# Performance work log

Measured on AMD Instinct MI355X. Metric: run time of the kernel, lower is better.

The kernel has to match this reference:

```python
import jax, jax.numpy as jnp
import numpy as np

B, DIM, N = 64, 128, 4000
H = 4
DH = DIM // H          # 32
CL = 50                # clusters (hardcoded in module)
K = 9                  # knn_num
SCALOR = DH ** -0.5


def setup_inputs() -> dict:
    key = jax.random.key(0)
    ks = jax.random.split(key, 16)
    s = 0.05
    inp = {
        'x': jax.random.normal(ks[0], (B, DIM, N, 1), jnp.float32),
        # conv_group1 / conv_group2: InstanceNorm(no affine) -> BN(affine) -> ReLU -> 1x1 conv
        'wg1': jax.random.normal(ks[1], (CL, DIM), jnp.float32) * s,
        'bg1': jnp.zeros((CL,), jnp.float32),
        'g1_gamma': jnp.ones((DIM,), jnp.float32),
        'g1_beta': jnp.zeros((DIM,), jnp.float32),
        'wg2': jax.random.normal(ks[2], (CL, DIM), jnp.float32) * s,
        'bg2': jnp.zeros((CL,), jnp.float32),
        'g2_gamma': jnp.ones((DIM,), jnp.float32),
        'g2_beta': jnp.zeros((DIM,), jnp.float32),
        # per-head 1x1 convs (stacked over heads)
        'qkv_w': jax.random.normal(ks[3], (H, DH, DIM), jnp.float32) * s,
        'qkv_b': jnp.zeros((H, DH), jnp.float32),
        'qkv1_w': jax.random.normal(ks[4], (H, 3 * DH, DIM), jnp.float32) * s,
        'qkv1_b': jnp.zeros((H, 3 * DH), jnp.float32),
        # GCBlock convs: conv1 (1,3) stride (1,3): 2*DH->DH ; conv2 (1,3): DH->DH
        'gc1_w': jax.random.normal(ks[5], (H, DH, 2 * DH, 3), jnp.float32) * s,
        'gc1_b': jnp.zeros((H, DH), jnp.float32),
        'gc1_gamma': jnp.ones((H, DH), jnp.float32),
        'gc1_beta': jnp.zeros((H, DH), jnp.float32),
        'gc2_w': jax.random.normal(ks[6], (H, DH, DH, 3), jnp.float32) * s,
        'gc2_b': jnp.zeros((H, DH), jnp.float32),
        'gc2_gamma': jnp.ones((H, DH), jnp.float32),
        'gc2_beta': jnp.zeros((H, DH), jnp.float32),
        # output projections
        'pres_w': jax.random.normal(ks[7], (DIM, 2 * DIM), jnp.float32) * s,
        'pres_b': jnp.zeros((DIM,), jnp.float32),
        'proj_w': jax.random.normal(ks[8], (DIM, DIM), jnp.float32) * s,
        'proj_b': jnp.zeros((DIM,), jnp.float32),
    }
    return inp


def _conv_group(x3, w, bconv, gamma, beta):
    # x3: (b, C, n). InstanceNorm2d(eps=1e-3, no affine) over n, BN(train) over (b,n), ReLU, 1x1 conv.
    mu = x3.mean(-1, keepdims=True)
    var = x3.var(-1, keepdims=True)
    xin = (x3 - mu) * jax.lax.rsqrt(var + 1e-3)
    mu2 = xin.mean((0, 2), keepdims=True)
    var2 = xin.var((0, 2), keepdims=True)
    xbn = gamma[None, :, None] * (xin - mu2) * jax.lax.rsqrt(var2 + 1e-5) + beta[None, :, None]
    xr = jax.nn.relu(xbn)
    return jnp.einsum('oc,bcn->bon', w, xr) + bconv[None, :, None]


def _bn_train(h, gamma, beta, axes):
    mu = h.mean(axes, keepdims=True)
    var = h.var(axes, keepdims=True)
    return gamma * (h - mu) * jax.lax.rsqrt(var + 1e-5) + beta


def _forward(x, wg1, bg1, g1_gamma, g1_beta, wg2, bg2, g2_gamma, g2_beta,
             qkv_w, qkv_b, qkv1_w, qkv1_b,
             gc1_w, gc1_b, gc1_gamma, gc1_beta,
             gc2_w, gc2_b, gc2_gamma, gc2_beta,
             pres_w, pres_b, proj_w, proj_b):
    xs = x[..., 0]                                          # (b, dim, n)
    # cluster assignment 1: softmax over points
    embed1 = _conv_group(xs, wg1, bg1, g1_gamma, g1_beta)   # (b, 50, n)
    S1 = jax.nn.softmax(embed1, axis=2)
    cluster_x = jnp.einsum('bdn,bcn->bdc', xs, S1)          # (b, dim, 50)

    # ---- local branch (per head, vectorized): 1x1 conv -> knn graph feature -> conv stack ----
    q = jnp.einsum('hod,bdc->bhoc', qkv_w, cluster_x) + qkv_b[None, :, :, None]  # (b,H,dh,50)
    xt = q.transpose(0, 1, 3, 2)                            # (b,H,50,dh)
    inner = jnp.einsum('bhnc,bhmc->bhnm', xt, xt)
    sq = jnp.sum(xt * xt, axis=-1)
    pd = 2.0 * inner - sq[..., :, None] - sq[..., None, :]  # negative squared distance
    idx = jax.lax.top_k(pd, K)[1]                            # (b,H,50,K)
    x_exp = jnp.broadcast_to(xt[:, :, None, :, :], xt.shape[:2] + (CL, CL, DH))
    feature = jnp.take_along_axis(x_exp, idx[..., None], axis=3)        # (b,H,50,K,dh)
    center = jnp.broadcast_to(xt[:, :, :, None, :], feature.shape)
    edge = jnp.concatenate([center, center - feature], axis=-1)          # (b,H,50,K,2dh)
    # conv1: kernel (1,3) stride (1,3): K=9 -> 3 windows of 3
    e = edge.reshape(edge.shape[0], H, CL, 3, 3, 2 * DH)
    h1 = jnp.einsum('bhnjti,hoit->bhnjo', e, gc1_w) + gc1_b[None, :, None, None, :]
    h1 = jax.nn.relu(_bn_train(h1, gc1_gamma[None, :, None, None, :], gc1_beta[None, :, None, None, :], (0, 2, 3)))
    # conv2: kernel (1,3): 3 -> 1
    h2 = jnp.einsum('bhnti,hoit->bhno', h1, gc2_w) + gc2_b[None, :, None, :]
    h2 = jax.nn.relu(_bn_train(h2, gc2_gamma[None, :, None, :], gc2_beta[None, :, None, :], (0, 2)))
    local = h2.transpose(0, 1, 3, 2)                        # (b,H,dh,50)

    # ---- global branch: tiny attention over 50 clusters per head ----
    qkv = jnp.einsum('hod,bdc->bhoc', qkv1_w, cluster_x) + qkv1_b[None, :, :, None]  # (b,H,3dh,50)
    qg, kg, vg = jnp.split(qkv, 3, axis=2)
    attn = jax.nn.softmax(SCALOR * jnp.einsum('bhdn,bhdm->bhnm', qg, kg), axis=-1)
    glob = jnp.einsum('bhnm,bhdm->bhdn', attn, vg)          # (b,H,dh,50)

    # interleave [local_h, global_h] per head along channels -> (b, 2*dim, 50)
    per_head = jnp.concatenate([local, glob], axis=2)       # (b,H,2dh,50)
    cat = per_head.reshape(per_head.shape[0], 2 * DIM, CL)
    res = jnp.einsum('oc,bcn->bon', pres_w, cat) + pres_b[None, :, None]  # (b,dim,50)

    # cluster assignment 2: softmax over clusters, scatter back to points
    embed2 = _conv_group(xs, wg2, bg2, g2_gamma, g2_beta)   # (b,50,n)
    S2 = jax.nn.softmax(embed2, axis=1)
    res2 = jnp.einsum('bdc,bcn->bdn', res, S2)              # (b,dim,n)
    out = jnp.einsum('od,bdn->bon', proj_w, res2) + proj_b[None, :, None]
    return out[..., None]                                   # (b,dim,n,1)


def reference(x, wg1, bg1, g1_gamma, g1_beta, wg2, bg2, g2_gamma, g2_beta,
              qkv_w, qkv_b, qkv1_w, qkv1_b,
              gc1_w, gc1_b, gc1_gamma, gc1_beta,
              gc2_w, gc2_b, gc2_gamma, gc2_beta,
              pres_w, pres_b, proj_w, proj_b):
    return _forward(x, wg1, bg1, g1_gamma, g1_beta, wg2, bg2, g2_gamma, g2_beta,
                    qkv_w, qkv_b, qkv1_w, qkv1_b,
                    gc1_w, gc1_b, gc1_gamma, gc1_beta,
                    gc2_w, gc2_b, gc2_gamma, gc2_beta,
                    pres_w, pres_b, proj_w, proj_b)
```

## Files before the change

### kernel.cpp

```cpp
#include <hip/hip_runtime.h>
#include <cstddef>


constexpr size_t O_MU    = 0;
constexpr size_t O_RINV  = 8192;
constexpr size_t O_RATIO = 16384;
constexpr size_t O_A1    = 24576;
constexpr size_t O_B1    = 24704;
constexpr size_t O_A2    = 24832;
constexpr size_t O_B2    = 24960;
constexpr size_t O_PROJWT= 25088;
constexpr size_t O_VPROJ = 41472;
constexpr size_t O_MT    = 41600;
constexpr size_t O_E2    = 74368;
constexpr size_t O_UCXP  = 12874368;
constexpr size_t O_XT    = 17068672;
constexpr size_t O_QT    = 17478272;
constexpr size_t O_KT    = 17887872;
constexpr size_t O_VT    = 18297472;
constexpr size_t O_H1    = 18707072;
constexpr size_t O_P1    = 19935872;
constexpr size_t O_H2    = 19952512;
constexpr size_t O_P2    = 20362112;
constexpr size_t O_CAT   = 20378752;
constexpr size_t O_PRES2 = 21197952;

__global__ __launch_bounds__(256) void k_rowstats(const float* __restrict__ x,
                                                  float* __restrict__ ws){
  int w = threadIdx.x >> 6, lane = threadIdx.x & 63;
  int row = blockIdx.x*4 + w;
  const float4* xr = (const float4*)(x + (size_t)row * 4000);
  float s = 0.f, sq = 0.f;
  for(int i = lane; i < 1000; i += 64){
    float4 v = xr[i];
    s  += v.x + v.y + v.z + v.w;
    sq += v.x*v.x + v.y*v.y + v.z*v.z + v.w*v.w;
  }
  for(int off = 32; off > 0; off >>= 1){
    s  += __shfl_down(s,  off, 64);
    sq += __shfl_down(sq, off, 64);
  }
  if(lane == 0){
    float mean = s * (1.f/4000.f);
    float var  = sq * (1.f/4000.f) - mean*mean;
    ws[O_MU   + row] = mean;
    ws[O_RINV + row] = rsqrtf(var + 1e-3f);
    ws[O_RATIO+ row] = var / (var + 1e-3f);
  }
}

__global__ __launch_bounds__(256) void k_prep(const float* g1g, const float* g1b,
                       const float* g2g, const float* g2b,
                       const float* projw, float* __restrict__ ws){
  int t = threadIdx.x;
  int i = blockIdx.x*256 + t;
  { int o = i & 127, k = i >> 7; ws[O_PROJWT+i] = projw[o*128 + k]; }
  if(blockIdx.x == 0 && t < 128){
    float s = 0.f;
    for(int b = 0; b < 64; b++) s += ws[O_RATIO + b*128 + t];
    float var2 = s * (1.f/64.f);
    float inv2 = rsqrtf(var2 + 1e-5f);
    ws[O_A1+t] = g1g[t] * inv2;  ws[O_B1+t] = g1b[t];
    ws[O_A2+t] = g2g[t] * inv2;  ws[O_B2+t] = g2b[t];
  }
}

__global__ __launch_bounds__(256) void k_mprep(const float* __restrict__ presw,
                                               const float* __restrict__ presb,
                                               float* __restrict__ ws){
  int t = threadIdx.x;
  if(blockIdx.x < 128){
    int kk2 = blockIdx.x * 2;
    __shared__ float pwc[2][128];
    { int which = t >> 7, d = t & 127; pwc[which][d] = presw[d*256 + kk2 + which]; }
    __syncthreads();
    int which = t >> 7, o = t & 127;
    float acc = 0.f;
    for(int d = 0; d < 128; d++) acc += ws[O_PROJWT + d*128 + o] * pwc[which][d];
    ws[O_MT + (size_t)(kk2 + which)*128 + o] = acc;
  }else{
    if(t < 128){
      float v = 0.f;
      for(int d = 0; d < 128; d++) v += ws[O_PROJWT + d*128 + t] * presb[d];
      ws[O_VPROJ + t] = v;
    }
  }
}

__global__ __launch_bounds__(256) void k_e1ucx(const float* __restrict__ x,
    const float* __restrict__ wg1, const float* __restrict__ bg1,
    float* __restrict__ ws){
  int ch = blockIdx.x, b = blockIdx.y;
  __shared__ float lW1[128*52];
  __shared__ float lrv1[128*48];
  __shared__ float lxt [48*132];
  __shared__ float ca1[128], cb1[128];
  __shared__ float bg1p[56];
  int t = threadIdx.x;
  if(t < 128){
    float mu = ws[O_MU + b*128 + t], ri = ws[O_RINV + b*128 + t];
    float a1 = ws[O_A1+t]*ri;
    ca1[t] = a1; cb1[t] = ws[O_B1+t] - a1*mu;
  }
  if(t < 56) bg1p[t] = (t < 50) ? bg1[t] : 0.f;
  for(int i = t; i < 1664; i += 256){
    int cl = i >> 5, cq = i & 31;
    float4 w = (cl < 50) ? *(const float4*)&wg1[cl*128 + cq*4] : make_float4(0.f,0.f,0.f,0.f);
    int c0 = cq*4;
    lW1[(c0+0)*52+cl] = w.x; lW1[(c0+1)*52+cl] = w.y;
    lW1[(c0+2)*52+cl] = w.z; lW1[(c0+3)*52+cl] = w.w;
  }
  int dg = t & 31, cg = t >> 5;
  float ua[4][8];
  #pragma unroll
  for(int r = 0; r < 4; r++)
    #pragma unroll
    for(int i = 0; i < 8; i++) ua[r][i] = 0.f;
  float zacc = 0.f;
  int ig = t >> 4, jg = t & 15;
  int clb = ig*4, j4 = jg*4;
  int sc[6], sj[6];
  float4 pf[6];
  #pragma unroll
  for(int j = 0; j < 6; j++){ int i = t + 256*j; sc[j] = i/12; sj[j] = (i%12)*4; }
  #pragma unroll
  for(int j = 0; j < 6; j++)
    pf[j] = *(const float4*)&x[(size_t)(b*128 + sc[j])*4000 + ch*500 + sj[j]];

  for(int st = 0; st < 11; st++){
    int lim = (st == 10) ? 20 : 48;
    __syncthreads();
    #pragma unroll
    for(int j = 0; j < 6; j++){
      int c = sc[j], jj = sj[j];
      float4 xv = (jj < lim) ? pf[j] : make_float4(0.f,0.f,0.f,0.f);
      lxt[(jj+0)*132 + c] = xv.x; lxt[(jj+1)*132 + c] = xv.y;
      lxt[(jj+2)*132 + c] = xv.z; lxt[(jj+3)*132 + c] = xv.w;
      float a1 = ca1[c], b1v = cb1[c];
      float4 r1;
      r1.x = fmaxf(a1*xv.x + b1v, 0.f); r1.y = fmaxf(a1*xv.y + b1v, 0.f);
      r1.z = fmaxf(a1*xv.z + b1v, 0.f); r1.w = fmaxf(a1*xv.w + b1v, 0.f);
      *(float4*)&lrv1[c*48 + jj] = r1;
    }
    __syncthreads();
    if(st < 10){
      int lim2 = (st == 9) ? 20 : 48;
      int nb2 = ch*500 + (st+1)*48;
      #pragma unroll
      for(int j = 0; j < 6; j++)
        pf[j] = (sj[j] < lim2) ? *(const float4*)&x[(size_t)(b*128 + sc[j])*4000 + nb2 + sj[j]]
                               : make_float4(0.f,0.f,0.f,0.f);
    }
    float e[4][4];
    if(ig < 13 && jg < 12){
      #pragma unroll
      for(int r = 0; r < 4; r++){ e[r][0]=0.f; e[r][1]=0.f; e[r][2]=0.f; e[r][3]=0.f; }
      #pragma unroll 4
      for(int c = 0; c < 128; c++){
        float4 w = *(const float4*)&lW1[c*52 + clb];
        float4 v = *(const float4*)&lrv1[c*48 + j4];
        e[0][0] += w.x*v.x; e[0][1] += w.x*v.y; e[0][2] += w.x*v.z; e[0][3] += w.x*v.w;
        e[1][0] += w.y*v.x; e[1][1] += w.y*v.y; e[1][2] += w.y*v.z; e[1][3] += w.y*v.w;
        e[2][0] += w.z*v.x; e[2][1] += w.z*v.y; e[2][2] += w.z*v.z; e[2][3] += w.z*v.w;
        e[3][0] += w.w*v.x; e[3][1] += w.w*v.y; e[3][2] += w.w*v.z; e[3][3] += w.w*v.w;
      }
    }
    __syncthreads();
    if(ig < 13 && jg < 12){
      bool live = (j4 < lim);
      #pragma unroll
      for(int r = 0; r < 4; r++){
        float bias = bg1p[clb + r];
        float4 u = make_float4(0.f,0.f,0.f,0.f);
        if(live){
          u.x = expf(e[r][0] + bias); u.y = expf(e[r][1] + bias);
          u.z = expf(e[r][2] + bias); u.w = expf(e[r][3] + bias);
        }
        *(float4*)&lrv1[(clb + r)*48 + j4] = u;
      }
    }
    __syncthreads();
    if(t < 224){
      int d4 = dg*4, c8 = cg*8;
      for(int n4 = 0; n4 < 12; n4++){
        int n0 = n4*4;
        float4 uv[8];
        #pragma unroll
        for(int i = 0; i < 8; i++) uv[i] = *(const float4*)&lrv1[(c8 + i)*48 + n0];
        {
          float4 xq = *(const float4*)&lxt[(n0+0)*132 + d4];
          #pragma unroll
          for(int i = 0; i < 8; i++){
            float u = uv[i].x;
            ua[0][i] += xq.x*u; ua[1][i] += xq.y*u; ua[2][i] += xq.z*u; ua[3][i] += xq.w*u;
          }
        }
        {
          float4 xq = *(const float4*)&lxt[(n0+1)*132 + d4];
          #pragma unroll
          for(int i = 0; i < 8; i++){
            float u = uv[i].y;
            ua[0][i] += xq.x*u; ua[1][i] += xq.y*u; ua[2][i] += xq.z*u; ua[3][i] += xq.w*u;
          }
        }
        {
          float4 xq = *(const float4*)&lxt[(n0+2)*132 + d4];
          #pragma unroll
          for(int i = 0; i < 8; i++){
            float u = uv[i].z;
            ua[0][i] += xq.x*u; ua[1][i] += xq.y*u; ua[2][i] += xq.z*u; ua[3][i] += xq.w*u;
          }
        }
        {
          float4 xq = *(const float4*)&lxt[(n0+3)*132 + d4];
          #pragma unroll
          for(int i = 0; i < 8; i++){
            float u = uv[i].w;
            ua[0][i] += xq.x*u; ua[1][i] += xq.y*u; ua[2][i] += xq.z*u; ua[3][i] += xq.w*u;
          }
        }
      }
    }
    if(t < 52){
      float s = 0.f;
      #pragma unroll
      for(int k = 0; k < 12; k++){
        float4 u = *(const float4*)&lrv1[t*48 + k*4];
        s += u.x + u.y + u.z + u.w;
      }
      zacc += s;
    }
  }
  if(t < 224){
    int d4 = dg*4, c8 = cg*8;
    #pragma unroll
    for(int r = 0; r < 4; r++){
      size_t base = O_UCXP + ((size_t)(ch*64 + b)*132 + d4 + r)*56 + c8;
      *(float4*)&ws[base]     = make_float4(ua[r][0], ua[r][1], ua[r][2], ua[r][3]);
      *(float4*)&ws[base + 4] = make_float4(ua[r][4], ua[r][5], ua[r][6], ua[r][7]);
    }
  }
  if(t < 52) ws[O_UCXP + ((size_t)(ch*64 + b)*132 + 128)*56 + t] = zacc;
}

__global__ __launch_bounds__(256) void k_e2(const float* __restrict__ x,
    const float* __restrict__ wg2, const float* __restrict__ bg2,
    float* __restrict__ ws){
  int ch = blockIdx.x, b = blockIdx.y;
  __shared__ float lW2[128*52];
  __shared__ float lrv2[128*48];
  __shared__ float ca2[128], cb2[128];
  __shared__ float bg2p[56];
  int t = threadIdx.x;
  if(t < 128){
    float mu = ws[O_MU + b*128 + t], ri = ws[O_RINV + b*128 + t];
    float a2 = ws[O_A2+t]*ri;
    ca2[t] = a2; cb2[t] = ws[O_B2+t] - a2*mu;
  }
  if(t < 56) bg2p[t] = (t < 50) ? bg2[t] : 0.f;
  for(int i = t; i < 1664; i += 256){
    int cl = i >> 5, cq = i & 31;
    float4 w = (cl < 50) ? *(const float4*)&wg2[cl*128 + cq*4] : make_float4(0.f,0.f,0.f,0.f);
    int c0 = cq*4;
    lW2[(c0+0)*52+cl] = w.x; lW2[(c0+1)*52+cl] = w.y;
    lW2[(c0+2)*52+cl] = w.z; lW2[(c0+3)*52+cl] = w.w;
  }
  int ig = t >> 4, jg = t & 15;
  int clb = ig*4, j4 = jg*4;
  int sc[6], sj[6];
  float4 pf[6];
  #pragma unroll
  for(int j = 0; j < 6; j++){ int i = t + 256*j; sc[j] = i/12; sj[j] = (i%12)*4; }
  #pragma unroll
  for(int j = 0; j < 6; j++)
    pf[j] = *(const float4*)&x[(size_t)(b*128 + sc[j])*4000 + ch*500 + sj[j]];

  for(int st = 0; st < 11; st++){
    int nb = ch*500 + st*48;
    int lim = (st == 10) ? 20 : 48;
    __syncthreads();
    #pragma unroll
    for(int j = 0; j < 6; j++){
      int c = sc[j], jj = sj[j];
      float4 xv = (jj < lim) ? pf[j] : make_float4(0.f,0.f,0.f,0.f);
      float a2 = ca2[c], b2v = cb2[c];
      float4 r2;
      r2.x = fmaxf(a2*xv.x + b2v, 0.f); r2.y = fmaxf(a2*xv.y + b2v, 0.f);
      r2.z = fmaxf(a2*xv.z + b2v, 0.f); r2.w = fmaxf(a2*xv.w + b2v, 0.f);
      *(float4*)&lrv2[c*48 + jj] = r2;
    }
    __syncthreads();
    if(st < 10){
      int lim2 = (st == 9) ? 20 : 48;
      int nb2 = ch*500 + (st+1)*48;
      #pragma unroll
      for(int j = 0; j < 6; j++)
        pf[j] = (sj[j] < lim2) ? *(const float4*)&x[(size_t)(b*128 + sc[j])*4000 + nb2 + sj[j]]
                               : make_float4(0.f,0.f,0.f,0.f);
    }
    if(ig < 13 && jg < 12){
      float e[4][4];
      #pragma unroll
      for(int r = 0; r < 4; r++){ e[r][0]=0.f; e[r][1]=0.f; e[r][2]=0.f; e[r][3]=0.f; }
      #pragma unroll 4
      for(int c = 0; c < 128; c++){
        float4 w = *(const float4*)&lW2[c*52 + clb];
        float4 v = *(const float4*)&lrv2[c*48 + j4];
        e[0][0] += w.x*v.x; e[0][1] += w.x*v.y; e[0][2] += w.x*v.z; e[0][3] += w.x*v.w;
        e[1][0] += w.y*v.x; e[1][1] += w.y*v.y; e[1][2] += w.y*v.z; e[1][3] += w.y*v.w;
        e[2][0] += w.z*v.x; e[2][1] += w.z*v.y; e[2][2] += w.z*v.z; e[2][3] += w.z*v.w;
        e[3][0] += w.w*v.x; e[3][1] += w.w*v.y; e[3][2] += w.w*v.z; e[3][3] += w.w*v.w;
      }
      if(j4 < lim){
        #pragma unroll
        for(int r = 0; r < 4; r++){
          int cl = clb + r;
          if(cl < 50){
            float bias = bg2p[cl];
            float4 o = make_float4(e[r][0]+bias, e[r][1]+bias, e[r][2]+bias, e[r][3]+bias);
            *(float4*)&ws[O_E2 + ((size_t)b*50 + cl)*4000 + nb + j4] = o;
          }
        }
      }
    }
  }
}

__global__ __launch_bounds__(256) void k_qkv(const float* __restrict__ qw,
                                             const float* __restrict__ qb,
                                             const float* __restrict__ q1w,
                                             const float* __restrict__ q1b,
                                             float* __restrict__ ws){
  int rt = blockIdx.x, b = blockIdx.y;
  __shared__ float wl[64*130];
  __shared__ float cxl[128*52];
  __shared__ float zi[52];
  int t = threadIdx.x;
  if(t < 52){
    float s = 0.f;
    if(t < 50){
      #pragma unroll
      for(int ch = 0; ch < 8; ch++)
        s += ws[O_UCXP + ((size_t)(ch*64 + b)*132 + 128)*56 + t];
      zi[t] = 1.f / s;
    }else zi[t] = 0.f;
  }
  for(int i = t; i < 2048; i += 256){
    int rl = i >> 5, kq = i & 31, row = rt*64 + rl;
    float4 w = (row < 128) ? *(const float4*)&qw[row*128 + kq*4]
                           : *(const float4*)&q1w[(row-128)*128 + kq*4];
    int k0 = kq*4;
    wl[rl*130 + k0+0] = w.x; wl[rl*130 + k0+1] = w.y;
    wl[rl*130 + k0+2] = w.z; wl[rl*130 + k0+3] = w.w;
  }
  __syncthreads();
  for(int i = t; i < 6656; i += 256){
    int k = i / 52, c = i % 52;
    float s = 0.f;
    size_t base = O_UCXP + ((size_t)b*132 + k)*56 + c;
    #pragma unroll
    for(int ch = 0; ch < 8; ch++) s += ws[base + (size_t)ch*64*132*56];
    cxl[i] = s * zi[c];
  }
  __syncthreads();
  int ig = t & 15, cg = t >> 4;
  float acc[4][4];
  #pragma unroll
  for(int r = 0; r < 4; r++){ acc[r][0]=0.f; acc[r][1]=0.f; acc[r][2]=0.f; acc[r][3]=0.f; }
  if(cg < 13){
    int rb = ig*4, cb = cg*4;
    #pragma unroll 4
    for(int k = 0; k < 128; k++){
      float4 cv = *(const float4*)&cxl[k*52 + cb];
      float w0 = wl[(rb+0)*130 + k], w1 = wl[(rb+1)*130 + k];
      float w2 = wl[(rb+2)*130 + k], w3 = wl[(rb+3)*130 + k];
      acc[0][0] += w0*cv.x; acc[0][1] += w0*cv.y; acc[0][2] += w0*cv.z; acc[0][3] += w0*cv.w;
      acc[1][0] += w1*cv.x; acc[1][1] += w1*cv.y; acc[1][2] += w1*cv.z; acc[1][3] += w1*cv.w;
      acc[2][0] += w2*cv.x; acc[2][1] += w2*cv.y; acc[2][2] += w2*cv.z; acc[2][3] += w2*cv.w;
      acc[3][0] += w3*cv.x; acc[3][1] += w3*cv.y; acc[3][2] += w3*cv.z; acc[3][3] += w3*cv.w;
    }
    #pragma unroll
    for(int r = 0; r < 4; r++){
      int row = rt*64 + ig*4 + r;
      size_t base; float bias;
      if(row < 128){
        int h = row >> 5;
        bias = qb[row];
        base = O_XT + (size_t)(b*4 + h)*1600 + (row & 31);
      }else{
        int r2 = row - 128, h = r2/96, j = r2%96, kind = j >> 5, dd = j & 31;
        bias = q1b[r2];
        base = (kind==0 ? O_QT : kind==1 ? O_KT : O_VT) + (size_t)(b*4 + h)*1600 + dd;
      }
      #pragma unroll
      for(int s = 0; s < 4; s++){
        int c = cg*4 + s;
        if(c < 50) ws[base + (size_t)c*32] = acc[r][s] + bias;
      }
    }
  }
}

__global__ __launch_bounds__(256) void k_knn(const float* __restrict__ g1w,
                                             const float* __restrict__ g1bias,
                                             float* __restrict__ ws){
  int h = blockIdx.x, b = blockIdx.y;
  __shared__ float xtl[50][33];
  __shared__ float pdl[50][52];
  __shared__ float sql[50];
  __shared__ int   idxl[50][9];
  __shared__ float w1l[6144];
  int t = threadIdx.x;
  const float* xtg = ws + O_XT + (size_t)(b*4 + h)*1600;
  for(int i = t; i < 1600; i += 256) xtl[i >> 5][i & 31] = xtg[i];
  for(int i = t; i < 6144; i += 256){
    int o = i / 192, r = i % 192, ii = r / 3, tt = r % 3;
    w1l[(ii*3 + tt)*32 + o] = g1w[(size_t)h*6144 + i];
  }
  __syncthreads();
  if(t < 50){
    float s = 0.f;
    for(int d = 0; d < 32; d++){ float v = xtl[t][d]; s += v*v; }
    sql[t] = s;
  }
  __syncthreads();
  for(int i = t; i < 2500; i += 256){
    int n = i / 50, m = i % 50;
    float s = 0.f;
    for(int d = 0; d < 32; d++) s += xtl[n][d]*xtl[m][d];
    pdl[n][m] = 2.f*s - sql[n] - sql[m];
  }
  __syncthreads();
  if(t < 50){
    float pv = INFINITY; int pi = -1;
    for(int k = 0; k < 9; k++){
      float bv = -INFINITY; int bi = 1000;
      for(int m = 0; m < 50; m++){
        float v = pdl[t][m];
        bool elig = (v < pv) || (v == pv && m > pi);
        if(elig && (v > bv || (v == bv && m < bi))){ bv = v; bi = m; }
      }
      idxl[t][k] = bi; pv = bv; pi = bi;
    }
  }
  __syncthreads();
  if(t < 150){
    int n = t / 3, jw = t % 3;
    float acc[32];
    #pragma unroll
    for(int o = 0; o < 32; o++) acc[o] = 0.f;
    for(int t3 = 0; t3 < 3; t3++){
      int kx = idxl[n][jw*3 + t3];
      for(int ii = 0; ii < 32; ii++){
        float c0 = xtl[n][ii];
        float c1 = c0 - xtl[kx][ii];
        const float* wr0 = w1l + (ii*3 + t3)*32;
        const float* wr1 = w1l + ((ii+32)*3 + t3)*32;
        #pragma unroll
        for(int o = 0; o < 32; o++) acc[o] += c0*wr0[o] + c1*wr1[o];
      }
    }
    float* out = ws + O_H1 + ((size_t)(b*4 + h)*150 + n*3 + jw)*32;
    #pragma unroll
    for(int o = 0; o < 32; o++) out[o] = acc[o] + g1bias[h*32 + o];
  }
}

__global__ __launch_bounds__(256) void k_bn1p(float* __restrict__ ws){
  int h = blockIdx.x, b = blockIdx.y, t = threadIdx.x;
  int o = t & 31, part = t >> 5;
  const float* src = ws + O_H1 + (size_t)(b*4 + h)*4800;
  float s = 0.f, sq = 0.f;
  for(int nj = part; nj < 150; nj += 8){
    float v = src[nj*32 + o];
    s += v; sq += v*v;
  }
  __shared__ float rs[8][33], rq[8][33];
  rs[part][o] = s; rq[part][o] = sq; __syncthreads();
  if(t < 32){
    float S = 0.f, Q = 0.f;
    for(int p = 0; p < 8; p++){ S += rs[p][t]; Q += rq[p][t]; }
    ws[O_P1 + b*256 + h*32 + t]       = S;
    ws[O_P1 + b*256 + 128 + h*32 + t] = Q;
  }
}

__global__ __launch_bounds__(256) void k_conv2(const float* __restrict__ g1g,
                                               const float* __restrict__ g1be,
                                               const float* __restrict__ g2w,
                                               const float* __restrict__ g2bias,
                                               float* __restrict__ ws){
  int h = blockIdx.x, b = blockIdx.y;
  __shared__ float hl[150][33];
  __shared__ float w2l[3072];
  __shared__ float rs[8][32], rq[8][32];
  __shared__ float b1s[32], b1t[32];
  int t = threadIdx.x;
  if(t < 32){
    float s = 0.f, sq = 0.f;
    for(int bb = 0; bb < 64; bb++){
      s  += ws[O_P1 + bb*256 + h*32 + t];
      sq += ws[O_P1 + bb*256 + 128 + h*32 + t];
    }
    float mean = s * (1.f/9600.f), var = sq * (1.f/9600.f) - mean*mean;
    float sc = g1g[h*32+t] * rsqrtf(var + 1e-5f);
    b1s[t] = sc; b1t[t] = g1be[h*32+t] - sc*mean;
  }
  for(int i = t; i < 3072; i += 256){
    int o = i / 96, r = i % 96, ii = r / 3, tt = r % 3;
    w2l[(ii*3 + tt)*32 + o] = g2w[(size_t)h*3072 + i];
  }
  __syncthreads();
  const float* h1p = ws + O_H1 + (size_t)(b*4 + h)*4800;
  for(int i = t; i < 4800; i += 256){
    int nj = i >> 5, ii = i & 31;
    hl[nj][ii] = fmaxf(b1s[ii]*h1p[i] + b1t[ii], 0.f);
  }
  __syncthreads();
  int o = t & 31, ng = t >> 5;
  float bias = g2bias[h*32 + o];
  float s = 0.f, sq = 0.f;
  for(int n = ng; n < 50; n += 8){
    float acc = 0.f;
    for(int t3 = 0; t3 < 3; t3++){
      const float* hr = hl[n*3 + t3];
      #pragma unroll
      for(int ii = 0; ii < 32; ii++) acc += hr[ii] * w2l[(ii*3 + t3)*32 + o];
    }
    acc += bias;
    ws[O_H2 + ((size_t)(b*4 + h)*50 + n)*32 + o] = acc;
    s += acc; sq += acc*acc;
  }
  rs[ng][o] = s; rq[ng][o] = sq; __syncthreads();
  if(t < 32){
    float S = 0.f, Q = 0.f;
    for(int g2 = 0; g2 < 8; g2++){ S += rs[g2][t]; Q += rq[g2][t]; }
    ws[O_P2 + (b*4 + h)*64 + t]      = S;
    ws[O_P2 + (b*4 + h)*64 + 32 + t] = Q;
  }
}

__global__ __launch_bounds__(256) void k_attn(const float* __restrict__ g2g,
                                              const float* __restrict__ g2be,
                                              float* __restrict__ ws){
  int h = blockIdx.x, b = blockIdx.y;
  __shared__ float qtl[50][33], ktl[50][33], vtl[50][33], al[50][52];
  __shared__ float b2s[32], b2t[32];
  int t = threadIdx.x;
  if(t < 32){
    float s = 0.f, sq = 0.f;
    for(int bb = 0; bb < 64; bb++){
      s  += ws[O_P2 + (size_t)(bb*4 + h)*64 + t];
      sq += ws[O_P2 + (size_t)(bb*4 + h)*64 + 32 + t];
    }
    float mean = s * (1.f/3200.f), var = sq * (1.f/3200.f) - mean*mean;
    float sc = g2g[h*32+t] * rsqrtf(var + 1e-5f);
    b2s[t] = sc; b2t[t] = g2be[h*32+t] - sc*mean;
  }
  size_t base = (size_t)(b*4 + h)*1600;
  for(int i = t; i < 1600; i += 256){
    int n = i >> 5, d = i & 31;
    qtl[n][d] = ws[O_QT + base + i];
    ktl[n][d] = ws[O_KT + base + i];
    vtl[n][d] = ws[O_VT + base + i];
  }
  __syncthreads();
  for(int i = t; i < 2500; i += 256){
    int n = i / 50, m = i % 50;
    float s = 0.f;
    for(int d = 0; d < 32; d++) s += qtl[n][d]*ktl[m][d];
    al[n][m] = s * 0.17677669529663687f;
  }
  __syncthreads();
  if(t < 50){
    float m = -INFINITY;
    for(int j = 0; j < 50; j++) m = fmaxf(m, al[t][j]);
    float s = 0.f;
    for(int j = 0; j < 50; j++){ float e = expf(al[t][j] - m); al[t][j] = e; s += e; }
    float inv = 1.f/s;
    for(int j = 0; j < 50; j++) al[t][j] *= inv;
  }
  __syncthreads();
  for(int i = t; i < 1600; i += 256){
    int n = i >> 5, d = i & 31;
    float gacc = 0.f;
    for(int m = 0; m < 50; m++) gacc += al[n][m]*vtl[m][d];
    ws[O_CAT + ((size_t)b*256 + h*64 + 32 + d)*50 + n] = gacc;
    float l = fmaxf(b2s[d]*ws[O_H2 + ((size_t)(b*4 + h)*50 + n)*32 + d] + b2t[d], 0.f);
    ws[O_CAT + ((size_t)b*256 + h*64 + d)*50 + n] = l;
  }
}

__global__ __launch_bounds__(256) void k_res(float* __restrict__ ws){
  int b = blockIdx.x;
  __shared__ float mtl[64*132];
  __shared__ float catl[64*52];
  __shared__ float vp[128];
  int t = threadIdx.x;
  if(t < 128) vp[t] = ws[O_VPROJ + t];
  int og = t >> 4, cg = t & 15;
  int ob = og*8, cb = cg*4;
  float acc[8][4];
  #pragma unroll
  for(int r = 0; r < 8; r++){ acc[r][0]=0.f; acc[r][1]=0.f; acc[r][2]=0.f; acc[r][3]=0.f; }
  for(int kc = 0; kc < 4; kc++){
    int k0 = kc*64;
    __syncthreads();
    for(int i = t; i < 2048; i += 256){
      int k = i >> 5, oq = i & 31;
      float4 m = *(const float4*)&ws[O_MT + (size_t)(k0 + k)*128 + oq*4];
      *(float4*)&mtl[k*132 + oq*4] = m;
    }
    for(int i = t; i < 3328; i += 256){
      int k = i / 52, c = i % 52;
      catl[i] = (c < 50) ? ws[O_CAT + (size_t)b*12800 + (k0 + k)*50 + c] : 0.f;
    }
    __syncthreads();
    if(cg < 13){
      #pragma unroll 2
      for(int k = 0; k < 64; k++){
        float4 m0 = *(const float4*)&mtl[k*132 + ob];
        float4 m1 = *(const float4*)&mtl[k*132 + ob + 4];
        float4 cv = *(const float4*)&catl[k*52 + cb];
        acc[0][0] += m0.x*cv.x; acc[0][1] += m0.x*cv.y; acc[0][2] += m0.x*cv.z; acc[0][3] += m0.x*cv.w;
        acc[1][0] += m0.y*cv.x; acc[1][1] += m0.y*cv.y; acc[1][2] += m0.y*cv.z; acc[1][3] += m0.y*cv.w;
        acc[2][0] += m0.z*cv.x; acc[2][1] += m0.z*cv.y; acc[2][2] += m0.z*cv.z; acc[2][3] += m0.z*cv.w;
        acc[3][0] += m0.w*cv.x; acc[3][1] += m0.w*cv.y; acc[3][2] += m0.w*cv.z; acc[3][3] += m0.w*cv.w;
        acc[4][0] += m1.x*cv.x; acc[4][1] += m1.x*cv.y; acc[4][2] += m1.x*cv.z; acc[4][3] += m1.x*cv.w;
        acc[5][0] += m1.y*cv.x; acc[5][1] += m1.y*cv.y; acc[5][2] += m1.y*cv.z; acc[5][3] += m1.y*cv.w;
        acc[6][0] += m1.z*cv.x; acc[6][1] += m1.z*cv.y; acc[6][2] += m1.z*cv.z; acc[6][3] += m1.z*cv.w;
        acc[7][0] += m1.w*cv.x; acc[7][1] += m1.w*cv.y; acc[7][2] += m1.w*cv.z; acc[7][3] += m1.w*cv.w;
      }
    }
  }
  if(cg < 13){
    #pragma unroll
    for(int s = 0; s < 4; s++){
      int c = cb + s;
      if(c < 50){
        float4 o0 = make_float4(acc[0][s]+vp[ob+0], acc[1][s]+vp[ob+1], acc[2][s]+vp[ob+2], acc[3][s]+vp[ob+3]);
        float4 o1 = make_float4(acc[4][s]+vp[ob+4], acc[5][s]+vp[ob+5], acc[6][s]+vp[ob+6], acc[7][s]+vp[ob+7]);
        *(float4*)&ws[O_PRES2 + (size_t)b*6400 + c*128 + ob]     = o0;
        *(float4*)&ws[O_PRES2 + (size_t)b*6400 + c*128 + ob + 4] = o1;
      }
    }
  }
}

__global__ __launch_bounds__(256) void k_out(const float* __restrict__ projb,
                                             float* __restrict__ ws,
                                             float* __restrict__ out){
  int nt = blockIdx.x, b = blockIdx.y;
  int n0 = nt*64;
  __shared__ float sl[50*64];
  __shared__ float p2l[50*132];
  __shared__ float pb[128];
  int t = threadIdx.x;
  for(int i = t; i < 3200; i += 256){
    int c = i >> 6, j = i & 63, n = n0 + j;
    sl[i] = (n < 4000) ? ws[O_E2 + ((size_t)b*50 + c)*4000 + n] : 0.f;
  }
  for(int i = t; i < 6400; i += 256){
    int c = i >> 7, o = i & 127;
    p2l[c*132 + o] = ws[O_PRES2 + (size_t)b*6400 + c*128 + o];
  }
  if(t < 128) pb[t] = projb[t];
  __syncthreads();
  if(t < 64){
    int j = t;
    float m = -INFINITY;
    for(int c = 0; c < 50; c++) m = fmaxf(m, sl[c*64 + j]);
    float s = 0.f;
    for(int c = 0; c < 50; c++){ float e = expf(sl[c*64 + j] - m); sl[c*64 + j] = e; s += e; }
    float inv = 1.f/s;
    for(int c = 0; c < 50; c++) sl[c*64 + j] *= inv;
  }
  __syncthreads();
  int og = t >> 4, jg = t & 15;
  int ob = og*8, j4 = jg*4;
  float acc[8][4];
  #pragma unroll
  for(int r = 0; r < 8; r++){ acc[r][0]=0.f; acc[r][1]=0.f; acc[r][2]=0.f; acc[r][3]=0.f; }
  #pragma unroll 2
  for(int c = 0; c < 50; c++){
    float4 sv = *(const float4*)&sl[c*64 + j4];
    float4 p0 = *(const float4*)&p2l[c*132 + ob];
    float4 p1 = *(const float4*)&p2l[c*132 + ob + 4];
    acc[0][0] += p0.x*sv.x; acc[0][1] += p0.x*sv.y; acc[0][2] += p0.x*sv.z; acc[0][3] += p0.x*sv.w;
    acc[1][0] += p0.y*sv.x; acc[1][1] += p0.y*sv.y; acc[1][2] += p0.y*sv.z; acc[1][3] += p0.y*sv.w;
    acc[2][0] += p0.z*sv.x; acc[2][1] += p0.z*sv.y; acc[2][2] += p0.z*sv.z; acc[2][3] += p0.z*sv.w;
    acc[3][0] += p0.w*sv.x; acc[3][1] += p0.w*sv.y; acc[3][2] += p0.w*sv.z; acc[3][3] += p0.w*sv.w;
    acc[4][0] += p1.x*sv.x; acc[4][1] += p1.x*sv.y; acc[4][2] += p1.x*sv.z; acc[4][3] += p1.x*sv.w;
    acc[5][0] += p1.y*sv.x; acc[5][1] += p1.y*sv.y; acc[5][2] += p1.y*sv.z; acc[5][3] += p1.y*sv.w;
    acc[6][0] += p1.z*sv.x; acc[6][1] += p1.z*sv.y; acc[6][2] += p1.z*sv.z; acc[6][3] += p1.z*sv.w;
    acc[7][0] += p1.w*sv.x; acc[7][1] += p1.w*sv.y; acc[7][2] += p1.w*sv.z; acc[7][3] += p1.w*sv.w;
  }
  int n = n0 + j4;
  if(n < 4000){
    #pragma unroll
    for(int r = 0; r < 8; r++){
      float bv = pb[ob + r];
      float4 o = make_float4(acc[r][0]+bv, acc[r][1]+bv, acc[r][2]+bv, acc[r][3]+bv);
      *(float4*)&out[(size_t)(b*128 + ob + r)*4000 + n] = o;
    }
  }
}

extern "C" void kernel_launch(void* const* d_in, const int* in_sizes, int n_in,
                              void* d_out, int out_size, void* d_ws, size_t ws_size,
                              hipStream_t stream){
  (void)in_sizes; (void)n_in; (void)out_size; (void)ws_size;
  const float* x      = (const float*)d_in[0];
  const float* wg1    = (const float*)d_in[1];
  const float* bg1    = (const float*)d_in[2];
  const float* g1g    = (const float*)d_in[3];
  const float* g1b    = (const float*)d_in[4];
  const float* wg2    = (const float*)d_in[5];
  const float* bg2    = (const float*)d_in[6];
  const float* g2g    = (const float*)d_in[7];
  const float* g2b    = (const float*)d_in[8];
  const float* qkvw   = (const float*)d_in[9];
  const float* qkvb   = (const float*)d_in[10];
  const float* qkv1w  = (const float*)d_in[11];
  const float* qkv1b  = (const float*)d_in[12];
  const float* gc1w   = (const float*)d_in[13];
  const float* gc1bias= (const float*)d_in[14];
  const float* gc1g   = (const float*)d_in[15];
  const float* gc1be  = (const float*)d_in[16];
  const float* gc2w   = (const float*)d_in[17];
  const float* gc2bias= (const float*)d_in[18];
  const float* gc2g   = (const float*)d_in[19];
  const float* gc2be  = (const float*)d_in[20];
  const float* presw  = (const float*)d_in[21];
  const float* presb  = (const float*)d_in[22];
  const float* projw  = (const float*)d_in[23];
  const float* projb  = (const float*)d_in[24];
  float* ws = (float*)d_ws;
  float* out = (float*)d_out;

  k_rowstats<<<2048, 256, 0, stream>>>(x, ws);
  k_prep<<<64, 256, 0, stream>>>(g1g, g1b, g2g, g2b, projw, ws);
  k_mprep<<<129, 256, 0, stream>>>(presw, presb, ws);
  k_e1ucx<<<dim3(8, 64), 256, 0, stream>>>(x, wg1, bg1, ws);
  k_e2<<<dim3(8, 64), 256, 0, stream>>>(x, wg2, bg2, ws);
  k_qkv<<<dim3(8, 64), 256, 0, stream>>>(qkvw, qkvb, qkv1w, qkv1b, ws);
  k_knn<<<dim3(4, 64), 256, 0, stream>>>(gc1w, gc1bias, ws);
  k_bn1p<<<dim3(4, 64), 256, 0, stream>>>(ws);
  k_conv2<<<dim3(4, 64), 256, 0, stream>>>(gc1g, gc1be, gc2w, gc2bias, ws);
  k_attn<<<dim3(4, 64), 256, 0, stream>>>(gc2g, gc2be, ws);
  k_res<<<64, 256, 0, stream>>>(ws);
  k_out<<<dim3(63, 64), 256, 0, stream>>>(projb, ws, out);
}
```

Baseline: 779.3 us.

## Fuse prep kernels, fold BN stats into knn, regrid e2 and res, skip softmax max

Merges the projw transpose into the row-stats kernel and the BN-scale prep into k_mprep. Folds the BN1 partial-stat reduction into k_knn, which removes one launch. Splits k_e2 across 12 chunks of 336 points with launch bounds for 3 blocks per SM, and splits k_res over two output halves to use more blocks. It also moves the exp into k_e2 and defers softmax normalization to the output GEMM, dropping the max-subtraction. That last step risks overflow if the logits grow large.

New measurement: 763.6 us. 2.0% less time.

```diff
diff --git a/kernel.cpp b/kernel.cpp
--- a/kernel.cpp
+++ b/kernel.cpp
@@ -14,19 +14,26 @@
 constexpr size_t O_MT    = 41600;
 constexpr size_t O_E2    = 74368;
 constexpr size_t O_UCXP  = 12874368;
-constexpr size_t O_XT    = 17068672;
-constexpr size_t O_QT    = 17478272;
-constexpr size_t O_KT    = 17887872;
-constexpr size_t O_VT    = 18297472;
-constexpr size_t O_H1    = 18707072;
-constexpr size_t O_P1    = 19935872;
-constexpr size_t O_H2    = 19952512;
-constexpr size_t O_P2    = 20362112;
-constexpr size_t O_CAT   = 20378752;
-constexpr size_t O_PRES2 = 21197952;
-
-__global__ __launch_bounds__(256) void k_rowstats(const float* __restrict__ x,
-                                                  float* __restrict__ ws){
+constexpr size_t O_XT    = 16659072;
+constexpr size_t O_QT    = 17068672;
+constexpr size_t O_KT    = 17478272;
+constexpr size_t O_VT    = 17887872;
+constexpr size_t O_H1    = 18297472;
+constexpr size_t O_P1    = 19526272;
+constexpr size_t O_H2    = 19542656;
+constexpr size_t O_P2    = 19952256;
+constexpr size_t O_CAT   = 19968640;
+constexpr size_t O_PRES2 = 20787840;
+
+__global__ __launch_bounds__(256) void k_stats(const float* __restrict__ x,
+                                               const float* __restrict__ projw,
+                                               float* __restrict__ ws){
+  if(blockIdx.x >= 2048){
+    int i = (blockIdx.x - 2048)*256 + threadIdx.x;
+    int o = i & 127, k = i >> 7;
+    ws[O_PROJWT + i] = projw[o*128 + k];
+    return;
+  }
   int w = threadIdx.x >> 6, lane = threadIdx.x & 63;
   int row = blockIdx.x*4 + w;
   const float4* xr = (const float4*)(x + (size_t)row * 4000);
@@ -49,24 +56,12 @@
   }
 }
 
-__global__ __launch_bounds__(256) void k_prep(const float* g1g, const float* g1b,
-                       const float* g2g, const float* g2b,
-                       const float* projw, float* __restrict__ ws){
-  int t = threadIdx.x;
-  int i = blockIdx.x*256 + t;
-  { int o = i & 127, k = i >> 7; ws[O_PROJWT+i] = projw[o*128 + k]; }
-  if(blockIdx.x == 0 && t < 128){
-    float s = 0.f;
-    for(int b = 0; b < 64; b++) s += ws[O_RATIO + b*128 + t];
-    float var2 = s * (1.f/64.f);
-    float inv2 = rsqrtf(var2 + 1e-5f);
-    ws[O_A1+t] = g1g[t] * inv2;  ws[O_B1+t] = g1b[t];
-    ws[O_A2+t] = g2g[t] * inv2;  ws[O_B2+t] = g2b[t];
-  }
-}
-
 __global__ __launch_bounds__(256) void k_mprep(const float* __restrict__ presw,
                                                const float* __restrict__ presb,
+                                               const float* __restrict__ g1g,
+                                               const float* __restrict__ g1b,
+                                               const float* __restrict__ g2g,
+                                               const float* __restrict__ g2b,
                                                float* __restrict__ ws){
   int t = threadIdx.x;
   if(blockIdx.x < 128){
@@ -78,11 +73,20 @@
     float acc = 0.f;
     for(int d = 0; d < 128; d++) acc += ws[O_PROJWT + d*128 + o] * pwc[which][d];
     ws[O_MT + (size_t)(kk2 + which)*128 + o] = acc;
-  }else{
+  }else if(blockIdx.x == 128){
     if(t < 128){
       float v = 0.f;
       for(int d = 0; d < 128; d++) v += ws[O_PROJWT + d*128 + t] * presb[d];
       ws[O_VPROJ + t] = v;
+    }
+  }else{
+    if(t < 128){
+      float s = 0.f;
+      for(int b = 0; b < 64; b++) s += ws[O_RATIO + b*128 + t];
+      float var2 = s * (1.f/64.f);
+      float inv2 = rsqrtf(var2 + 1e-5f);
+      ws[O_A1+t] = g1g[t] * inv2;  ws[O_B1+t] = g1b[t];
+      ws[O_A2+t] = g2g[t] * inv2;  ws[O_B2+t] = g2b[t];
     }
   }
 }
@@ -243,7 +247,7 @@
   if(t < 52) ws[O_UCXP + ((size_t)(ch*64 + b)*132 + 128)*56 + t] = zacc;
 }
 
-__global__ __launch_bounds__(256) void k_e2(const float* __restrict__ x,
+__global__ __launch_bounds__(256, 3) void k_e2(const float* __restrict__ x,
     const float* __restrict__ wg2, const float* __restrict__ bg2,
     float* __restrict__ ws){
   int ch = blockIdx.x, b = blockIdx.y;
@@ -257,7 +261,7 @@
     float a2 = ws[O_A2+t]*ri;
     ca2[t] = a2; cb2[t] = ws[O_B2+t] - a2*mu;
   }
-  if(t < 56) bg2p[t] = (t < 50) ? bg2[t] : 0.f;
+  if(t >= 192 && t < 248){ int q = t - 192; bg2p[q] = (q < 50) ? bg2[q] : 0.f; }
   for(int i = t; i < 1664; i += 256){
     int cl = i >> 5, cq = i & 31;
     float4 w = (cl < 50) ? *(const float4*)&wg2[cl*128 + cq*4] : make_float4(0.f,0.f,0.f,0.f);
@@ -273,11 +277,11 @@
   for(int j = 0; j < 6; j++){ int i = t + 256*j; sc[j] = i/12; sj[j] = (i%12)*4; }
   #pragma unroll
   for(int j = 0; j < 6; j++)
-    pf[j] = *(const float4*)&x[(size_t)(b*128 + sc[j])*4000 + ch*500 + sj[j]];
-
-  for(int st = 0; st < 11; st++){
-    int nb = ch*500 + st*48;
-    int lim = (st == 10) ? 20 : 48;
+    pf[j] = *(const float4*)&x[(size_t)(b*128 + sc[j])*4000 + ch*336 + sj[j]];
+
+  for(int st = 0; st < 7; st++){
+    int nb = ch*336 + st*48;
+    int lim = 4000 - nb; if(lim > 48) lim = 48;
     __syncthreads();
     #pragma unroll
     for(int j = 0; j < 6; j++){
@@ -290,9 +294,9 @@
       *(float4*)&lrv2[c*48 + jj] = r2;
     }
     __syncthreads();
-    if(st < 10){
-      int lim2 = (st == 9) ? 20 : 48;
-      int nb2 = ch*500 + (st+1)*48;
+    if(st < 6){
+      int nb2 = nb + 48;
+      int lim2 = 4000 - nb2; if(lim2 > 48) lim2 = 48;
       #pragma unroll
       for(int j = 0; j < 6; j++)
         pf[j] = (sj[j] < lim2) ? *(const float4*)&x[(size_t)(b*128 + sc[j])*4000 + nb2 + sj[j]]
@@ -317,7 +321,8 @@
           int cl = clb + r;
           if(cl < 50){
             float bias = bg2p[cl];
-            float4 o = make_float4(e[r][0]+bias, e[r][1]+bias, e[r][2]+bias, e[r][3]+bias);
+            float4 o = make_float4(expf(e[r][0]+bias), expf(e[r][1]+bias),
+                                   expf(e[r][2]+bias), expf(e[r][3]+bias));
             *(float4*)&ws[O_E2 + ((size_t)b*50 + cl)*4000 + nb + j4] = o;
           }
         }
@@ -359,7 +364,7 @@
     float s = 0.f;
     size_t base = O_UCXP + ((size_t)b*132 + k)*56 + c;
     #pragma unroll
-    for(int ch = 0; ch < 8; ch++) s += ws[base + (size_t)ch*64*132*56];
+    for(int ch = 0; ch < 8; ch++) s += ws[base + (size_t)ch*473088];
     cxl[i] = s * zi[c];
   }
   __syncthreads();
@@ -444,9 +449,10 @@
     }
   }
   __syncthreads();
-  if(t < 150){
+  float acc[32];
+  bool act = (t < 150);
+  if(act){
     int n = t / 3, jw = t % 3;
-    float acc[32];
     #pragma unroll
     for(int o = 0; o < 32; o++) acc[o] = 0.f;
     for(int t3 = 0; t3 < 3; t3++){
@@ -462,26 +468,30 @@
     }
     float* out = ws + O_H1 + ((size_t)(b*4 + h)*150 + n*3 + jw)*32;
     #pragma unroll
-    for(int o = 0; o < 32; o++) out[o] = acc[o] + g1bias[h*32 + o];
-  }
-}
-
-__global__ __launch_bounds__(256) void k_bn1p(float* __restrict__ ws){
-  int h = blockIdx.x, b = blockIdx.y, t = threadIdx.x;
-  int o = t & 31, part = t >> 5;
-  const float* src = ws + O_H1 + (size_t)(b*4 + h)*4800;
-  float s = 0.f, sq = 0.f;
-  for(int nj = part; nj < 150; nj += 8){
-    float v = src[nj*32 + o];
-    s += v; sq += v*v;
-  }
-  __shared__ float rs[8][33], rq[8][33];
-  rs[part][o] = s; rq[part][o] = sq; __syncthreads();
-  if(t < 32){
-    float S = 0.f, Q = 0.f;
-    for(int p = 0; p < 8; p++){ S += rs[p][t]; Q += rq[p][t]; }
-    ws[O_P1 + b*256 + h*32 + t]       = S;
-    ws[O_P1 + b*256 + 128 + h*32 + t] = Q;
+    for(int o = 0; o < 32; o++){ acc[o] += g1bias[h*32 + o]; out[o] = acc[o]; }
+  }
+  __syncthreads();
+  if(act){
+    #pragma unroll
+    for(int o = 0; o < 32; o++) w1l[t*32 + o] = acc[o];
+  }
+  __syncthreads();
+  {
+    int o = t & 31, part = t >> 5;
+    float s = 0.f, sq = 0.f;
+    for(int r = part; r < 150; r += 8){
+      float v = w1l[r*32 + o];
+      s += v; sq += v*v;
+    }
+    float* sp = &pdl[0][0];
+    sp[part*32 + o] = s; sp[256 + part*32 + o] = sq;
+    __syncthreads();
+    if(t < 32){
+      float S = 0.f, Q = 0.f;
+      for(int p = 0; p < 8; p++){ S += sp[p*32 + t]; Q += sp[256 + p*32 + t]; }
+      ws[O_P1 + b*256 + h*32 + t]       = S;
+      ws[O_P1 + b*256 + 128 + h*32 + t] = Q;
+    }
   }
 }
 
@@ -546,6 +556,7 @@
   int h = blockIdx.x, b = blockIdx.y;
   __shared__ float qtl[50][33], ktl[50][33], vtl[50][33], al[50][52];
   __shared__ float b2s[32], b2t[32];
+  __shared__ float zr[50];
   int t = threadIdx.x;
   if(t < 32){
     float s = 0.f, sq = 0.f;
@@ -577,39 +588,38 @@
     for(int j = 0; j < 50; j++) m = fmaxf(m, al[t][j]);
     float s = 0.f;
     for(int j = 0; j < 50; j++){ float e = expf(al[t][j] - m); al[t][j] = e; s += e; }
-    float inv = 1.f/s;
-    for(int j = 0; j < 50; j++) al[t][j] *= inv;
+    zr[t] = 1.f/s;
   }
   __syncthreads();
   for(int i = t; i < 1600; i += 256){
     int n = i >> 5, d = i & 31;
     float gacc = 0.f;
     for(int m = 0; m < 50; m++) gacc += al[n][m]*vtl[m][d];
-    ws[O_CAT + ((size_t)b*256 + h*64 + 32 + d)*50 + n] = gacc;
+    ws[O_CAT + ((size_t)b*256 + h*64 + 32 + d)*50 + n] = gacc * zr[n];
     float l = fmaxf(b2s[d]*ws[O_H2 + ((size_t)(b*4 + h)*50 + n)*32 + d] + b2t[d], 0.f);
     ws[O_CAT + ((size_t)b*256 + h*64 + d)*50 + n] = l;
   }
 }
 
 __global__ __launch_bounds__(256) void k_res(float* __restrict__ ws){
-  int b = blockIdx.x;
-  __shared__ float mtl[64*132];
+  int oh = blockIdx.x & 1, b = blockIdx.x >> 1;
+  __shared__ float mtl[64*68];
   __shared__ float catl[64*52];
-  __shared__ float vp[128];
-  int t = threadIdx.x;
-  if(t < 128) vp[t] = ws[O_VPROJ + t];
+  __shared__ float vp[64];
+  int t = threadIdx.x;
+  if(t < 64) vp[t] = ws[O_VPROJ + oh*64 + t];
   int og = t >> 4, cg = t & 15;
-  int ob = og*8, cb = cg*4;
-  float acc[8][4];
+  int ob = og*4, cb = cg*4;
+  float acc[4][4];
   #pragma unroll
-  for(int r = 0; r < 8; r++){ acc[r][0]=0.f; acc[r][1]=0.f; acc[r][2]=0.f; acc[r][3]=0.f; }
+  for(int r = 0; r < 4; r++){ acc[r][0]=0.f; acc[r][1]=0.f; acc[r][2]=0.f; acc[r][3]=0.f; }
   for(int kc = 0; kc < 4; kc++){
     int k0 = kc*64;
     __syncthreads();
-    for(int i = t; i < 2048; i += 256){
-      int k = i >> 5, oq = i & 31;
-      float4 m = *(const float4*)&ws[O_MT + (size_t)(k0 + k)*128 + oq*4];
-      *(float4*)&mtl[k*132 + oq*4] = m;
+    for(int i = t; i < 1024; i += 256){
+      int k = i >> 4, oq = i & 15;
+      float4 m = *(const float4*)&ws[O_MT + (size_t)(k0 + k)*128 + oh*64 + oq*4];
+      *(float4*)&mtl[k*68 + oq*4] = m;
     }
     for(int i = t; i < 3328; i += 256){
       int k = i / 52, c = i % 52;
@@ -619,17 +629,12 @@
     if(cg < 13){
       #pragma unroll 2
       for(int k = 0; k < 64; k++){
-        float4 m0 = *(const float4*)&mtl[k*132 + ob];
-        float4 m1 = *(const float4*)&mtl[k*132 + ob + 4];
+        float4 m0 = *(const float4*)&mtl[k*68 + ob];
         float4 cv = *(const float4*)&catl[k*52 + cb];
         acc[0][0] += m0.x*cv.x; acc[0][1] += m0.x*cv.y; acc[0][2] += m0.x*cv.z; acc[0][3] += m0.x*cv.w;
         acc[1][0] += m0.y*cv.x; acc[1][1] += m0.y*cv.y; acc[1][2] += m0.y*cv.z; acc[1][3] += m0.y*cv.w;
         acc[2][0] += m0.z*cv.x; acc[2][1] += m0.z*cv.y; acc[2][2] += m0.z*cv.z; acc[2][3] += m0.z*cv.w;
         acc[3][0] += m0.w*cv.x; acc[3][1] += m0.w*cv.y; acc[3][2] += m0.w*cv.z; acc[3][3] += m0.w*cv.w;
-        acc[4][0] += m1.x*cv.x; acc[4][1] += m1.x*cv.y; acc[4][2] += m1.x*cv.z; acc[4][3] += m1.x*cv.w;
-        acc[5][0] += m1.y*cv.x; acc[5][1] += m1.y*cv.y; acc[5][2] += m1.y*cv.z; acc[5][3] += m1.y*cv.w;
-        acc[6][0] += m1.z*cv.x; acc[6][1] += m1.z*cv.y; acc[6][2] += m1.z*cv.z; acc[6][3] += m1.z*cv.w;
-        acc[7][0] += m1.w*cv.x; acc[7][1] += m1.w*cv.y; acc[7][2] += m1.w*cv.z; acc[7][3] += m1.w*cv.w;
       }
     }
   }
@@ -639,9 +644,7 @@
       int c = cb + s;
       if(c < 50){
         float4 o0 = make_float4(acc[0][s]+vp[ob+0], acc[1][s]+vp[ob+1], acc[2][s]+vp[ob+2], acc[3][s]+vp[ob+3]);
-        float4 o1 = make_float4(acc[4][s]+vp[ob+4], acc[5][s]+vp[ob+5], acc[6][s]+vp[ob+6], acc[7][s]+vp[ob+7]);
-        *(float4*)&ws[O_PRES2 + (size_t)b*6400 + c*128 + ob]     = o0;
-        *(float4*)&ws[O_PRES2 + (size_t)b*6400 + c*128 + ob + 4] = o1;
+        *(float4*)&ws[O_PRES2 + (size_t)b*6400 + c*128 + oh*64 + ob] = o0;
       }
     }
   }
@@ -655,6 +658,8 @@
   __shared__ float sl[50*64];
   __shared__ float p2l[50*132];
   __shared__ float pb[128];
+  __shared__ float zp[4][64];
+  __shared__ float zi[64];
   int t = threadIdx.x;
   for(int i = t; i < 3200; i += 256){
     int c = i >> 6, j = i & 63, n = n0 + j;
@@ -666,15 +671,14 @@
   }
   if(t < 128) pb[t] = projb[t];
   __syncthreads();
-  if(t < 64){
-    int j = t;
-    float m = -INFINITY;
-    for(int c = 0; c < 50; c++) m = fmaxf(m, sl[c*64 + j]);
+  {
+    int j = t & 63, q = t >> 6;
     float s = 0.f;
-    for(int c = 0; c < 50; c++){ float e = expf(sl[c*64 + j] - m); sl[c*64 + j] = e; s += e; }
-    float inv = 1.f/s;
-    for(int c = 0; c < 50; c++) sl[c*64 + j] *= inv;
-  }
+    for(int c = q; c < 50; c += 4) s += sl[c*64 + j];
+    zp[q][j] = s;
+  }
+  __syncthreads();
+  if(t < 64) zi[t] = 1.f / (zp[0][t] + zp[1][t] + zp[2][t] + zp[3][t]);
   __syncthreads();
   int og = t >> 4, jg = t & 15;
   int ob = og*8, j4 = jg*4;
@@ -697,10 +701,11 @@
   }
   int n = n0 + j4;
   if(n < 4000){
+    float z0 = zi[j4+0], z1 = zi[j4+1], z2 = zi[j4+2], z3 = zi[j4+3];
     #pragma unroll
     for(int r = 0; r < 8; r++){
       float bv = pb[ob + r];
-      float4 o = make_float4(acc[r][0]+bv, acc[r][1]+bv, acc[r][2]+bv, acc[r][3]+bv);
+      float4 o = make_float4(acc[r][0]*z0+bv, acc[r][1]*z1+bv, acc[r][2]*z2+bv, acc[r][3]*z3+bv);
       *(float4*)&out[(size_t)(b*128 + ob + r)*4000 + n] = o;
     }
   }
@@ -738,16 +743,14 @@
   float* ws = (float*)d_ws;
   float* out = (float*)d_out;
 
-  k_rowstats<<<2048, 256, 0, stream>>>(x, ws);
-  k_prep<<<64, 256, 0, stream>>>(g1g, g1b, g2g, g2b, projw, ws);
-  k_mprep<<<129, 256, 0, stream>>>(presw, presb, ws);
+  k_stats<<<2112, 256, 0, stream>>>(x, projw, ws);
+  k_mprep<<<130, 256, 0, stream>>>(presw, presb, g1g, g1b, g2g, g2b, ws);
   k_e1ucx<<<dim3(8, 64), 256, 0, stream>>>(x, wg1, bg1, ws);
-  k_e2<<<dim3(8, 64), 256, 0, stream>>>(x, wg2, bg2, ws);
+  k_e2<<<dim3(12, 64), 256, 0, stream>>>(x, wg2, bg2, ws);
   k_qkv<<<dim3(8, 64), 256, 0, stream>>>(qkvw, qkvb, qkv1w, qkv1b, ws);
   k_knn<<<dim3(4, 64), 256, 0, stream>>>(gc1w, gc1bias, ws);
-  k_bn1p<<<dim3(4, 64), 256, 0, stream>>>(ws);
   k_conv2<<<dim3(4, 64), 256, 0, stream>>>(gc1g, gc1be, gc2w, gc2bias, ws);
   k_attn<<<dim3(4, 64), 256, 0, stream>>>(gc2g, gc2be, ws);
-  k_res<<<64, 256, 0, stream>>>(ws);
+  k_res<<<128, 256, 0, stream>>>(ws);
   k_out<<<dim3(63, 64), 256, 0, stream>>>(projb, ws, out);
 }
```
